# Performance work log

Hardware: AMD Instinct MI355X
Metric: run time of the kernel (lower is better)

## Reference

```python
import jax, jax.numpy as jnp
from jax import lax
import numpy as np

NUM_GROUP = 512
GROUP_SIZE = 32
BIG = jnp.float32(1e10)


def _fps_single(pts, num_group):
    # pts: [N, 3] -> indices [G] via farthest point sampling, starting at index 0
    N = pts.shape[0]

    def step(carry, _):
        dists, farthest = carry
        centroid = pts[farthest]                       # [3]
        d = jnp.sum((pts - centroid) ** 2, axis=-1)    # [N]
        dists = jnp.minimum(dists, d)
        nxt = jnp.argmax(dists).astype(jnp.int32)
        return (dists, nxt), farthest

    init = (jnp.full((N,), BIG, dtype=pts.dtype), jnp.int32(0))
    _, idxs = lax.scan(step, init, None, length=num_group)
    return idxs  # [G] int32


def setup_inputs() -> dict:
    key = jax.random.key(0)
    xyz = jax.random.normal(key, (8, 8192, 6), dtype=jnp.float32)
    return {"xyz": xyz}


def reference(xyz):
    # xyz: [B, N, 6]
    B, N, _ = xyz.shape
    xyz_only = xyz[:, :, :3]        # [B, N, 3]
    attr_only = xyz[:, :, 3:]       # [B, N, A]

    # --- FPS: sample NUM_GROUP centers per batch ---
    fps_idx = jax.vmap(_fps_single, in_axes=(0, None))(xyz_only, NUM_GROUP)  # [B, G]
    center = jnp.take_along_axis(xyz_only, fps_idx[:, :, None], axis=1)      # [B, G, 3]
    center_attribute = jnp.take_along_axis(attr_only, fps_idx[:, :, None], axis=1)  # [B, G, A]

    # --- KNN: GROUP_SIZE nearest points to each center ---
    # squared dist [B, G, N] = |c|^2 - 2 c.p + |p|^2
    d2 = (jnp.sum(center ** 2, -1)[:, :, None]
          - 2.0 * jnp.einsum('bgc,bnc->bgn', center, xyz_only)
          + jnp.sum(xyz_only ** 2, -1)[:, None, :])
    _, idx = lax.top_k(-d2, GROUP_SIZE)   # [B, G, K]

    # --- gather neighborhoods and center xyz ---
    gather = jax.vmap(lambda p, i: p[i])  # per-batch gather: [N,C], [G,K] -> [G,K,C]
    neigh_xyz = gather(xyz_only, idx) - center[:, :, None, :]   # [B, G, K, 3]
    neigh_attr = gather(attr_only, idx)                          # [B, G, K, A]

    return (neigh_xyz, neigh_attr, center, center_attribute)
```

## Files before the change

### kernel.cpp

```cpp
#include <hip/hip_runtime.h>
#include <stdint.h>

#define N_PTS 8192
#define N_B 8
#define NGROUP 512
#define GSIZE 32
#define BIGF 1e10f

#define THREADS 512
#define TOT_BLOCKS 256
#define FPS_BLOCKS 8
#define KNN_BLOCKS (TOT_BLOCKS - FPS_BLOCKS)

#define K1_PPT 16
#define K1_WAVES 8

#define K2_PPT 16
#define K2_WAVES 8

#define FMAX3(a, b, c) fmaxf(fmaxf((a), (b)), (c))

#define DPP_STEP_UMIN(ctrl, rmask)                                                 \
    { unsigned t = (unsigned)__builtin_amdgcn_update_dpp(                          \
            (int)v, (int)v, ctrl, rmask, 0xF, false);                              \
      v = (t < v) ? t : v; }

__device__ __forceinline__ unsigned wave_umin32(unsigned v) {
    DPP_STEP_UMIN(0x111, 0xF);
    DPP_STEP_UMIN(0x112, 0xF);
    DPP_STEP_UMIN(0x114, 0xF);
    DPP_STEP_UMIN(0x118, 0xF);
    DPP_STEP_UMIN(0x142, 0xA);
    DPP_STEP_UMIN(0x143, 0xC);
    return v;
}

#define DPP_STEP_FMAX(ctrl, rmask)                                                 \
    v = fmaxf(v, __int_as_float(__builtin_amdgcn_update_dpp(                       \
            __float_as_int(v), __float_as_int(v), ctrl, rmask, 0xF, false)))

__device__ __forceinline__ float wave_fmax(float v) {
    DPP_STEP_FMAX(0x111, 0xF);
    DPP_STEP_FMAX(0x112, 0xF);
    DPP_STEP_FMAX(0x114, 0xF);
    DPP_STEP_FMAX(0x118, 0xF);
    DPP_STEP_FMAX(0x142, 0xA);
    DPP_STEP_FMAX(0x143, 0xC);
    return v;
}

#define U64_DPP_STEP(ctrl, rmask, CMPOP)                                           \
    { unsigned lo_ = (unsigned)v, hi_ = (unsigned)(v >> 32);                       \
      unsigned olo = (unsigned)__builtin_amdgcn_update_dpp((int)lo_, (int)lo_, ctrl, rmask, 0xF, false); \
      unsigned ohi = (unsigned)__builtin_amdgcn_update_dpp((int)hi_, (int)hi_, ctrl, rmask, 0xF, false); \
      unsigned long long o = ((unsigned long long)ohi << 32) | olo;                \
      if (o CMPOP v) v = o; }

__device__ __forceinline__ int rdlane63_i(int v) {
    return __builtin_amdgcn_readlane(v, 63);
}

__device__ __forceinline__ unsigned fxform(unsigned u) {
    return u ^ (unsigned)(((int)u >> 31) | 0x80000000);
}

template<int N>
__device__ __forceinline__ void bitonic_sort(unsigned long long* a) {
#pragma unroll
    for (int k = 2; k <= N; k <<= 1) {
#pragma unroll
        for (int j = k >> 1; j > 0; j >>= 1) {
#pragma unroll
            for (int i = 0; i < N; ++i) {
                int ixj = i ^ j;
                if (ixj > i) {
                    bool up = ((i & k) == 0);
                    unsigned long long x = a[i], y = a[ixj];
                    bool sw = up ? (x > y) : (x < y);
                    if (sw) { a[i] = y; a[ixj] = x; }
                }
            }
        }
    }
}

union SharedLDS {
    struct {
        float lx[N_PTS]; float ly[N_PTS]; float lz[N_PTS];
        unsigned long long part[2][K1_WAVES];
    } f;
    struct {
        unsigned long long wtop[K2_WAVES][GSIZE];
        unsigned nlist[GSIZE];
        int qshare;
    } k;
};

extern "C" __global__ __launch_bounds__(THREADS, 1) void fused_kernel(
    const float* __restrict__ xyz, float* __restrict__ out,
    int* __restrict__ fps_idx)
{
    __shared__ SharedLDS S;
    const int bid = blockIdx.x;
    const int tid = threadIdx.x;
    const int lane = tid & 63;
    const int wid  = tid >> 6;

    if (bid < FPS_BLOCKS) {
        const int b = bid;
        const float* base = xyz + (size_t)b * N_PTS * 6;
        const float4* b4 = (const float4*)base;

        typedef float v2f __attribute__((ext_vector_type(2)));
        v2f px[8], py[8], pz[8];
        float dd[K1_PPT];

        const int tb = tid * 24;
#pragma unroll
        for (int c = 0; c < 4; ++c) {
            float4 f0 = b4[tb + c * 6 + 0];
            float4 f1 = b4[tb + c * 6 + 1];
            float4 f2 = b4[tb + c * 6 + 2];
            float4 f3 = b4[tb + c * 6 + 3];
            float4 f4 = b4[tb + c * 6 + 4];
            float4 f5 = b4[tb + c * 6 + 5];
            px[c * 2 + 0] = (v2f){f0.x, f1.z};
            py[c * 2 + 0] = (v2f){f0.y, f1.w};
            pz[c * 2 + 0] = (v2f){f0.z, f2.x};
            px[c * 2 + 1] = (v2f){f3.x, f4.z};
            py[c * 2 + 1] = (v2f){f3.y, f4.w};
            pz[c * 2 + 1] = (v2f){f3.z, f5.x};
        }
#pragma unroll
        for (int i = 0; i < K1_PPT; ++i) {
            int a = (i << 9) + tid;
            S.f.lx[a] = px[i >> 1][i & 1];
            S.f.ly[a] = py[i >> 1][i & 1];
            S.f.lz[a] = pz[i >> 1][i & 1];
            dd[i] = BIGF;
        }
        __syncthreads();

        unsigned cur = 0;
        float cx = S.f.lx[0], cy = S.f.ly[0], cz = S.f.lz[0];

        for (int it = 0; it < NGROUP; ++it) {
            if (tid == 0) {
                __hip_atomic_store(&fps_idx[b * NGROUP + it], (int)cur,
                                   __ATOMIC_RELAXED, __HIP_MEMORY_SCOPE_AGENT);
            }
            if (it == NGROUP - 1) break;

            {
#pragma clang fp contract(off)
                v2f c2x = {cx, cx};
                v2f c2y = {cy, cy};
                v2f c2z = {cz, cz};
#pragma unroll
                for (int q = 0; q < 8; ++q) {
                    v2f dx = px[q] - c2x;
                    v2f dy = py[q] - c2y;
                    v2f dz = pz[q] - c2z;
                    v2f s  = (dx * dx + dy * dy) + dz * dz;
                    dd[2 * q + 0] = fminf(dd[2 * q + 0], s[0]);
                    dd[2 * q + 1] = fminf(dd[2 * q + 1], s[1]);
                }
            }

            float t0 = FMAX3(dd[0],  dd[1],  dd[2]);
            float t1 = FMAX3(dd[3],  dd[4],  dd[5]);
            float t2 = FMAX3(dd[6],  dd[7],  dd[8]);
            float t3 = FMAX3(dd[9],  dd[10], dd[11]);
            float t4 = FMAX3(dd[12], dd[13], dd[14]);
            float bestd = fmaxf(FMAX3(t0, t1, t2), FMAX3(t3, t4, dd[15]));
            unsigned besti = 0;
#pragma unroll
            for (int i = K1_PPT - 1; i >= 0; --i)
                besti = (dd[i] == bestd) ? (unsigned)i : besti;

            unsigned bestp = (unsigned)tid * K1_PPT + besti;

            float wm = __int_as_float(rdlane63_i(__float_as_int(wave_fmax(bestd))));
            unsigned long long bal = __ballot(bestd == wm);
            int L = (int)(__ffsll((long long)bal) - 1);
            unsigned widx = (unsigned)__builtin_amdgcn_readlane((int)bestp, L);

            if (lane == 0) {
                S.f.part[it & 1][wid] =
                    ((unsigned long long)__float_as_uint(wm) << 32) |
                    (unsigned long long)(0xFFFFFFFFu - widx);
            }

            asm volatile("s_waitcnt lgkmcnt(0)" ::: "memory");
            __builtin_amdgcn_s_barrier();
            __builtin_amdgcn_sched_barrier(0);

            unsigned long long v = S.f.part[it & 1][lane & 7];
            U64_DPP_STEP(0x111, 0xF, >);
            U64_DPP_STEP(0x112, 0xF, >);
            U64_DPP_STEP(0x114, 0xF, >);
            unsigned wkl = (unsigned)__builtin_amdgcn_readlane((int)(unsigned)v, 7);
            cur = 0xFFFFFFFFu - wkl;

            int wa = (int)(((cur & 15u) << 9) + (cur >> 4));
            cx = S.f.lx[wa];
            cy = S.f.ly[wa];
            cz = S.f.lz[wa];
        }
        return;
    }

    const int OFF1 = N_B * NGROUP * GSIZE * 3;
    const int OFF2 = 2 * OFF1;
    const int OFF3 = OFF2 + N_B * NGROUP * 3;

    for (int idx = bid - FPS_BLOCKS; idx < N_B * NGROUP; idx += KNN_BLOCKS) {
        const int g = idx >> 3;
        const int b = idx & 7;
        const float* base = xyz + (size_t)b * N_PTS * 6;

        if (tid == 0) {
            int qv;
            while ((qv = __hip_atomic_load(&fps_idx[b * NGROUP + g], __ATOMIC_RELAXED,
                                           __HIP_MEMORY_SCOPE_AGENT)) < 0)
                __builtin_amdgcn_s_sleep(32);
            S.k.qshare = qv;
        }
        __syncthreads();

        const int qq = __builtin_amdgcn_readfirstlane(S.k.qshare);
        const float cx = base[qq * 6 + 0];
        const float cy = base[qq * 6 + 1];
        const float cz = base[qq * 6 + 2];
        const float cn = __fadd_rn(__fadd_rn(__fmul_rn(cx, cx), __fmul_rn(cy, cy)),
                                   __fmul_rn(cz, cz));

        const float4* b4 = (const float4*)base;
        const int tb = tid * 24;

        unsigned long long keys[K2_PPT];

#pragma unroll
        for (int c = 0; c < 4; ++c) {
            float4 f0 = b4[tb + c * 6 + 0];
            float4 f1 = b4[tb + c * 6 + 1];
            float4 f2 = b4[tb + c * 6 + 2];
            float4 f3 = b4[tb + c * 6 + 3];
            float4 f4 = b4[tb + c * 6 + 4];
            float4 f5 = b4[tb + c * 6 + 5];
            float X[4] = {f0.x, f1.z, f3.x, f4.z};
            float Y[4] = {f0.y, f1.w, f3.y, f4.w};
            float Z[4] = {f0.z, f2.x, f3.z, f5.x};
#pragma unroll
            for (int j = 0; j < 4; ++j) {
                float x = X[j], y = Y[j], z = Z[j];
                float xn  = __fadd_rn(__fadd_rn(__fmul_rn(x, x), __fmul_rn(y, y)), __fmul_rn(z, z));
                float dot = __fmul_rn(cx, x);
                dot = __fmaf_rn(cy, y, dot);
                dot = __fmaf_rn(cz, z, dot);
                float d2  = __fadd_rn(__fsub_rn(cn, __fmul_rn(2.0f, dot)), xn);
                int p = tid * K2_PPT + c * 4 + j;
                keys[c * 4 + j] =
                    ((unsigned long long)fxform(__float_as_uint(d2)) << 32) | (unsigned)p;
            }
        }

        bitonic_sort<K2_PPT>(keys);

        {
            unsigned long long cand = keys[0];
            unsigned w = 0;
            for (int r = 0; r < GSIZE; ++r) {
                unsigned ch = (unsigned)(cand >> 32);
                unsigned whd = (unsigned)rdlane63_i((int)wave_umin32(ch));
                unsigned long long bal = __ballot(ch == whd);
                unsigned wl;
                if (__popcll(bal) == 1) {
                    int L = (int)(__ffsll((long long)bal) - 1);
                    wl = (unsigned)__builtin_amdgcn_readlane((int)(unsigned)cand, L);
                } else {
                    unsigned cl = (ch == whd) ? (unsigned)cand : 0xFFFFFFFFu;
                    wl = (unsigned)rdlane63_i((int)wave_umin32(cl));
                }
                unsigned long long wkey = ((unsigned long long)whd << 32) | wl;
                if (lane == 0) S.k.wtop[wid][r] = wkey;
                if (cand == wkey) {
                    ++w;
                    unsigned long long nc;
                    if (w < 4) {
                        nc = (w == 1) ? keys[1] : (w == 2) ? keys[2] : keys[3];
                    } else if (w < K2_PPT) {
                        nc = keys[4];
#pragma unroll
                        for (int j = 5; j < K2_PPT; ++j) nc = (w == (unsigned)j) ? keys[j] : nc;
                    } else {
                        nc = ~0ull;
                    }
                    cand = nc;
                }
            }
        }
        __syncthreads();

        if (tid < K2_WAVES * GSIZE) {
            const int w8 = tid >> 5, i = tid & 31;
            unsigned long long e = S.k.wtop[w8][i];
            int rank = 0;
#pragma unroll
            for (int l = 0; l < K2_WAVES; ++l) {
                const unsigned long long* arr = S.k.wtop[l];
                int lo = 0;
                if (arr[15]     < e) lo = 16;
                if (arr[lo + 7] < e) lo += 8;
                if (arr[lo + 3] < e) lo += 4;
                if (arr[lo + 1] < e) lo += 2;
                if (arr[lo]     < e) lo += 1;
                rank += lo;
            }
            if (rank < GSIZE) S.k.nlist[rank] = (unsigned)e;
        }
        __syncthreads();

        if (tid < GSIZE) {
            unsigned p = S.k.nlist[tid];
            float x  = base[p * 6 + 0];
            float y  = base[p * 6 + 1];
            float z  = base[p * 6 + 2];
            float a0 = base[p * 6 + 3];
            float a1 = base[p * 6 + 4];
            float a2 = base[p * 6 + 5];
            size_t o = ((size_t)(b * NGROUP + g) * GSIZE + tid) * 3;
            out[o + 0] = __fsub_rn(x, cx);
            out[o + 1] = __fsub_rn(y, cy);
            out[o + 2] = __fsub_rn(z, cz);
            out[OFF1 + o + 0] = a0;
            out[OFF1 + o + 1] = a1;
            out[OFF1 + o + 2] = a2;
        } else if (tid == GSIZE) {
            size_t o = (size_t)(b * NGROUP + g) * 3;
            out[OFF2 + o + 0] = cx;
            out[OFF2 + o + 1] = cy;
            out[OFF2 + o + 2] = cz;
            out[OFF3 + o + 0] = base[qq * 6 + 3];
            out[OFF3 + o + 1] = base[qq * 6 + 4];
            out[OFF3 + o + 2] = base[qq * 6 + 5];
        }
    }
}

extern "C" void kernel_launch(void* const* d_in, const int* in_sizes, int n_in,
                              void* d_out, int out_size, void* d_ws, size_t ws_size,
                              hipStream_t stream) {
    const float* xyz = (const float*)d_in[0];
    float* out = (float*)d_out;
    int* fps_idx = (int*)d_ws;

    fused_kernel<<<TOT_BLOCKS, THREADS, 0, stream>>>(xyz, out, fps_idx);
}
```

Baseline: 529.0 us.

## Process two batches per FPS block and carry winner coordinates through partial records

Each FPS block now runs farthest point sampling for two batches at once, interleaving their updates so both share one barrier per iteration. This halves the number of FPS blocks and frees blocks for KNN work. The per-wave candidate record now carries the candidate's xyz, read from global memory, so the point cloud no longer needs to be staged in LDS and the post-barrier LDS coordinate lookup goes away. In exchange, each wave does twice the work and uses twice the registers per iteration, which lengthens the serial FPS critical path per iteration, and every iteration issues global loads.

```diff
diff --git a/kernel.cpp b/kernel.cpp
--- a/kernel.cpp
+++ b/kernel.cpp
@@ -9,7 +9,7 @@
 
 #define THREADS 512
 #define TOT_BLOCKS 256
-#define FPS_BLOCKS 8
+#define FPS_BLOCKS 4
 #define KNN_BLOCKS (TOT_BLOCKS - FPS_BLOCKS)
 
 #define K1_PPT 16
@@ -19,6 +19,8 @@
 #define K2_WAVES 8
 
 #define FMAX3(a, b, c) fmaxf(fmaxf((a), (b)), (c))
+
+typedef float v2f __attribute__((ext_vector_type(2)));
 
 #define DPP_STEP_UMIN(ctrl, rmask)                                                 \
     { unsigned t = (unsigned)__builtin_amdgcn_update_dpp(                          \
@@ -84,10 +86,12 @@
     }
 }
 
+struct __align__(32) PartRec { unsigned long long key; float x, y, z; };
+
 union SharedLDS {
     struct {
-        float lx[N_PTS]; float ly[N_PTS]; float lz[N_PTS];
-        unsigned long long part[2][K1_WAVES];
+        PartRec pA[2][K1_WAVES];
+        PartRec pB[2][K1_WAVES];
     } f;
     struct {
         unsigned long long wtop[K2_WAVES][GSIZE];
@@ -95,6 +99,72 @@
         int qshare;
     } k;
 };
+
+__device__ __forceinline__ void fps_update(const v2f* px, const v2f* py, const v2f* pz,
+                                           float* dd, float cx, float cy, float cz,
+                                           float& bestd_o, unsigned& besti_o)
+{
+    {
+#pragma clang fp contract(off)
+        v2f c2x = {cx, cx};
+        v2f c2y = {cy, cy};
+        v2f c2z = {cz, cz};
+#pragma unroll
+        for (int q = 0; q < 8; ++q) {
+            v2f dx = px[q] - c2x;
+            v2f dy = py[q] - c2y;
+            v2f dz = pz[q] - c2z;
+            v2f s  = (dx * dx + dy * dy) + dz * dz;
+            dd[2 * q + 0] = fminf(dd[2 * q + 0], s[0]);
+            dd[2 * q + 1] = fminf(dd[2 * q + 1], s[1]);
+        }
+    }
+    float t0 = FMAX3(dd[0],  dd[1],  dd[2]);
+    float t1 = FMAX3(dd[3],  dd[4],  dd[5]);
+    float t2 = FMAX3(dd[6],  dd[7],  dd[8]);
+    float t3 = FMAX3(dd[9],  dd[10], dd[11]);
+    float t4 = FMAX3(dd[12], dd[13], dd[14]);
+    float bestd = fmaxf(FMAX3(t0, t1, t2), FMAX3(t3, t4, dd[15]));
+    unsigned besti = 0;
+#pragma unroll
+    for (int i = K1_PPT - 1; i >= 0; --i)
+        besti = (dd[i] == bestd) ? (unsigned)i : besti;
+    bestd_o = bestd;
+    besti_o = besti;
+}
+
+__device__ __forceinline__ void fps_wave_phase(float bestd, unsigned pid,
+                                               const float* __restrict__ base,
+                                               PartRec* slot, int lane)
+{
+    const float sx = base[pid * 6 + 0];
+    const float sy = base[pid * 6 + 1];
+    const float sz = base[pid * 6 + 2];
+    float wm = __int_as_float(rdlane63_i(__float_as_int(wave_fmax(bestd))));
+    unsigned long long bal = __ballot(bestd == wm);
+    int L = (int)(__ffsll((long long)bal) - 1);
+    if (lane == L) {
+        slot->key = ((unsigned long long)__float_as_uint(wm) << 32)
+                  | (unsigned long long)(0xFFFFFFFFu - pid);
+        slot->x = sx; slot->y = sy; slot->z = sz;
+    }
+}
+
+__device__ __forceinline__ void fps_reduce(const PartRec* rec,
+                                           unsigned& cur, float& cx, float& cy, float& cz)
+{
+    unsigned long long v = rec->key;
+    float rx = rec->x, ry = rec->y, rz = rec->z;
+    U64_DPP_STEP(0x111, 0xF, >);
+    U64_DPP_STEP(0x112, 0xF, >);
+    U64_DPP_STEP(0x114, 0xF, >);
+    unsigned wkl = (unsigned)__builtin_amdgcn_readlane((int)(unsigned)v, 7);
+    cur = 0xFFFFFFFFu - wkl;
+    int W = (int)(cur >> 10);
+    cx = __int_as_float(__builtin_amdgcn_readlane(__float_as_int(rx), W));
+    cy = __int_as_float(__builtin_amdgcn_readlane(__float_as_int(ry), W));
+    cz = __int_as_float(__builtin_amdgcn_readlane(__float_as_int(rz), W));
+}
 
 extern "C" __global__ __launch_bounds__(THREADS, 1) void fused_kernel(
     const float* __restrict__ xyz, float* __restrict__ out,
@@ -107,15 +177,32 @@
     const int wid  = tid >> 6;
 
     if (bid < FPS_BLOCKS) {
-        const int b = bid;
-        const float* base = xyz + (size_t)b * N_PTS * 6;
-        const float4* b4 = (const float4*)base;
-
-        typedef float v2f __attribute__((ext_vector_type(2)));
-        v2f px[8], py[8], pz[8];
-        float dd[K1_PPT];
+        const int bA = 2 * bid, bB = 2 * bid + 1;
+        const float* baseA = xyz + (size_t)bA * N_PTS * 6;
+        const float* baseB = xyz + (size_t)bB * N_PTS * 6;
+        const float4* a4 = (const float4*)baseA;
+        const float4* b4 = (const float4*)baseB;
+
+        v2f pax[8], pay[8], paz[8];
+        v2f pbx[8], pby[8], pbz[8];
+        float ddA[K1_PPT], ddB[K1_PPT];
 
         const int tb = tid * 24;
+#pragma unroll
+        for (int c = 0; c < 4; ++c) {
+            float4 f0 = a4[tb + c * 6 + 0];
+            float4 f1 = a4[tb + c * 6 + 1];
+            float4 f2 = a4[tb + c * 6 + 2];
+            float4 f3 = a4[tb + c * 6 + 3];
+            float4 f4 = a4[tb + c * 6 + 4];
+            float4 f5 = a4[tb + c * 6 + 5];
+            pax[c * 2 + 0] = (v2f){f0.x, f1.z};
+            pay[c * 2 + 0] = (v2f){f0.y, f1.w};
+            paz[c * 2 + 0] = (v2f){f0.z, f2.x};
+            pax[c * 2 + 1] = (v2f){f3.x, f4.z};
+            pay[c * 2 + 1] = (v2f){f3.y, f4.w};
+            paz[c * 2 + 1] = (v2f){f3.z, f5.x};
+        }
 #pragma unroll
         for (int c = 0; c < 4; ++c) {
             float4 f0 = b4[tb + c * 6 + 0];
@@ -124,88 +211,50 @@
             float4 f3 = b4[tb + c * 6 + 3];
             float4 f4 = b4[tb + c * 6 + 4];
             float4 f5 = b4[tb + c * 6 + 5];
-            px[c * 2 + 0] = (v2f){f0.x, f1.z};
-            py[c * 2 + 0] = (v2f){f0.y, f1.w};
-            pz[c * 2 + 0] = (v2f){f0.z, f2.x};
-            px[c * 2 + 1] = (v2f){f3.x, f4.z};
-            py[c * 2 + 1] = (v2f){f3.y, f4.w};
-            pz[c * 2 + 1] = (v2f){f3.z, f5.x};
-        }
-#pragma unroll
-        for (int i = 0; i < K1_PPT; ++i) {
-            int a = (i << 9) + tid;
-            S.f.lx[a] = px[i >> 1][i & 1];
-            S.f.ly[a] = py[i >> 1][i & 1];
-            S.f.lz[a] = pz[i >> 1][i & 1];
-            dd[i] = BIGF;
-        }
-        __syncthreads();
-
-        unsigned cur = 0;
-        float cx = S.f.lx[0], cy = S.f.ly[0], cz = S.f.lz[0];
-
-        for (int it = 0; it < NGROUP; ++it) {
-            if (tid == 0) {
-                __hip_atomic_store(&fps_idx[b * NGROUP + it], (int)cur,
-                                   __ATOMIC_RELAXED, __HIP_MEMORY_SCOPE_AGENT);
-            }
-            if (it == NGROUP - 1) break;
-
-            {
-#pragma clang fp contract(off)
-                v2f c2x = {cx, cx};
-                v2f c2y = {cy, cy};
-                v2f c2z = {cz, cz};
-#pragma unroll
-                for (int q = 0; q < 8; ++q) {
-                    v2f dx = px[q] - c2x;
-                    v2f dy = py[q] - c2y;
-                    v2f dz = pz[q] - c2z;
-                    v2f s  = (dx * dx + dy * dy) + dz * dz;
-                    dd[2 * q + 0] = fminf(dd[2 * q + 0], s[0]);
-                    dd[2 * q + 1] = fminf(dd[2 * q + 1], s[1]);
-                }
-            }
-
-            float t0 = FMAX3(dd[0],  dd[1],  dd[2]);
-            float t1 = FMAX3(dd[3],  dd[4],  dd[5]);
-            float t2 = FMAX3(dd[6],  dd[7],  dd[8]);
-            float t3 = FMAX3(dd[9],  dd[10], dd[11]);
-            float t4 = FMAX3(dd[12], dd[13], dd[14]);
-            float bestd = fmaxf(FMAX3(t0, t1, t2), FMAX3(t3, t4, dd[15]));
-            unsigned besti = 0;
-#pragma unroll
-            for (int i = K1_PPT - 1; i >= 0; --i)
-                besti = (dd[i] == bestd) ? (unsigned)i : besti;
-
-            unsigned bestp = (unsigned)tid * K1_PPT + besti;
-
-            float wm = __int_as_float(rdlane63_i(__float_as_int(wave_fmax(bestd))));
-            unsigned long long bal = __ballot(bestd == wm);
-            int L = (int)(__ffsll((long long)bal) - 1);
-            unsigned widx = (unsigned)__builtin_amdgcn_readlane((int)bestp, L);
-
-            if (lane == 0) {
-                S.f.part[it & 1][wid] =
-                    ((unsigned long long)__float_as_uint(wm) << 32) |
-                    (unsigned long long)(0xFFFFFFFFu - widx);
-            }
+            pbx[c * 2 + 0] = (v2f){f0.x, f1.z};
+            pby[c * 2 + 0] = (v2f){f0.y, f1.w};
+            pbz[c * 2 + 0] = (v2f){f0.z, f2.x};
+            pbx[c * 2 + 1] = (v2f){f3.x, f4.z};
+            pby[c * 2 + 1] = (v2f){f3.y, f4.w};
+            pbz[c * 2 + 1] = (v2f){f3.z, f5.x};
+        }
+#pragma unroll
+        for (int i = 0; i < K1_PPT; ++i) { ddA[i] = BIGF; ddB[i] = BIGF; }
+
+        float cAx = baseA[0], cAy = baseA[1], cAz = baseA[2];
+        float cBx = baseB[0], cBy = baseB[1], cBz = baseB[2];
+        unsigned curA = 0, curB = 0;
+
+        if (tid == 0) {
+            __hip_atomic_store(&fps_idx[bA * NGROUP + 0], 0,
+                               __ATOMIC_RELAXED, __HIP_MEMORY_SCOPE_AGENT);
+            __hip_atomic_store(&fps_idx[bB * NGROUP + 0], 0,
+                               __ATOMIC_RELAXED, __HIP_MEMORY_SCOPE_AGENT);
+        }
+
+        for (int it = 0; it < NGROUP - 1; ++it) {
+            float bestdA, bestdB; unsigned bestiA, bestiB;
+            fps_update(pax, pay, paz, ddA, cAx, cAy, cAz, bestdA, bestiA);
+            fps_update(pbx, pby, pbz, ddB, cBx, cBy, cBz, bestdB, bestiB);
+
+            fps_wave_phase(bestdA, (unsigned)tid * K1_PPT + bestiA, baseA,
+                           &S.f.pA[it & 1][wid], lane);
+            fps_wave_phase(bestdB, (unsigned)tid * K1_PPT + bestiB, baseB,
+                           &S.f.pB[it & 1][wid], lane);
 
             asm volatile("s_waitcnt lgkmcnt(0)" ::: "memory");
             __builtin_amdgcn_s_barrier();
             __builtin_amdgcn_sched_barrier(0);
 
-            unsigned long long v = S.f.part[it & 1][lane & 7];
-            U64_DPP_STEP(0x111, 0xF, >);
-            U64_DPP_STEP(0x112, 0xF, >);
-            U64_DPP_STEP(0x114, 0xF, >);
-            unsigned wkl = (unsigned)__builtin_amdgcn_readlane((int)(unsigned)v, 7);
-            cur = 0xFFFFFFFFu - wkl;
-
-            int wa = (int)(((cur & 15u) << 9) + (cur >> 4));
-            cx = S.f.lx[wa];
-            cy = S.f.ly[wa];
-            cz = S.f.lz[wa];
+            fps_reduce(&S.f.pA[it & 1][lane & 7], curA, cAx, cAy, cAz);
+            fps_reduce(&S.f.pB[it & 1][lane & 7], curB, cBx, cBy, cBz);
+
+            if (tid == 0) {
+                __hip_atomic_store(&fps_idx[bA * NGROUP + it + 1], (int)curA,
+                                   __ATOMIC_RELAXED, __HIP_MEMORY_SCOPE_AGENT);
+                __hip_atomic_store(&fps_idx[bB * NGROUP + it + 1], (int)curB,
+                                   __ATOMIC_RELAXED, __HIP_MEMORY_SCOPE_AGENT);
+            }
         }
         return;
     }
```

Result: slower. 996.3 us (+88.3%).
